# Kernel tuning notes

Hardware: AMD Instinct MI355X
Metric: run time of the kernel (lower is better)

Reference implementation:

```python
import jax, jax.numpy as jnp
import numpy as np

WINDOW_SIZE = 11
SIGMA = 1.5
C_IN = 3

def _gaussian_window():
    coords = jnp.arange(WINDOW_SIZE, dtype=jnp.float32) - WINDOW_SIZE // 2
    g = jnp.exp(-(coords ** 2) / (2.0 * SIGMA ** 2))
    g = g / g.sum()
    win = g[:, None] * g[None, :]                       # [11, 11]
    return jnp.broadcast_to(win[None, None], (C_IN, 1, WINDOW_SIZE, WINDOW_SIZE))

def _depthwise_conv(x, w):
    pad = WINDOW_SIZE // 2
    return jax.lax.conv_general_dilated(
        x, w,
        window_strides=(1, 1),
        padding=[(pad, pad), (pad, pad)],
        dimension_numbers=('NCHW', 'OIHW', 'NCHW'),
        feature_group_count=C_IN)

def setup_inputs() -> dict:
    key = jax.random.key(0)
    k1, k2 = jax.random.split(key)
    clean = jax.random.uniform(k1, (32, 3, 512, 512), dtype=jnp.float32)
    adversarial = jax.random.uniform(k2, (32, 3, 512, 512), dtype=jnp.float32)
    return {"clean": clean, "adversarial": adversarial}

def reference(clean, adversarial):
    C1 = 0.01 ** 2
    C2 = 0.03 ** 2
    w = _gaussian_window()
    mu1 = _depthwise_conv(clean, w)
    mu2 = _depthwise_conv(adversarial, w)
    mu1_sq = mu1 ** 2
    mu2_sq = mu2 ** 2
    mu12 = mu1 * mu2
    sigma1_sq = _depthwise_conv(clean ** 2, w) - mu1_sq
    sigma2_sq = _depthwise_conv(adversarial ** 2, w) - mu2_sq
    sigma12 = _depthwise_conv(clean * adversarial, w) - mu12
    ssim_map = ((2.0 * mu12 + C1) * (2.0 * sigma12 + C2)) / (
        (mu1_sq + mu2_sq + C1) * (sigma1_sq + sigma2_sq + C2))
    return 1.0 - ssim_map.mean()
```

## Files before the change

### kernel.cpp

```cpp
#include <hip/hip_runtime.h>


typedef float v2f __attribute__((ext_vector_type(2)));

#define IMG 512
#define TILE 64
#define HALO 5
#define LROWS 74
#define LCOLS 74
#define LSTRIDE 76
#define RPT 8
#define NPIX 25165824.0

__device__ __constant__ const float WT_[1] = {0.f};
#define W0 0.00102838f
#define W1 0.00759876f
#define W2 0.03600077f
#define W3 0.10936068f
#define W4 0.21300552f
#define W5 0.26601173f
__device__ constexpr float WT[11] = {W0, W1, W2, W3, W4, W5, W4, W3, W2, W1, W0};

__global__ __launch_bounds__(256, 3) void ssim_main(
    const float* __restrict__ clean,
    const float* __restrict__ adv,
    double* __restrict__ accum)
{
    __shared__ __align__(16) v2f tile[LROWS * LSTRIDE];
    __shared__ float wpart[4];

    const int tid = threadIdx.x;
    const int b = blockIdx.x;
    const int plane = b >> 6;
    const int t6 = b & 63;
    const int tile_x = (t6 & 7) * TILE;
    const int tile_y = (t6 >> 3) * TILE;

    const float* __restrict__ cp = clean + (size_t)plane * (IMG * IMG);
    const float* __restrict__ ap = adv   + (size_t)plane * (IMG * IMG);

    for (int idx = tid; idx < LROWS * LCOLS; idx += 256) {
        int r = idx / LCOLS;
        int c = idx - r * LCOLS;
        int gr = tile_y + r - HALO;
        int gc = tile_x + c - HALO;
        v2f v = {0.f, 0.f};
        if (gr >= 0 && gr < IMG && gc >= 0 && gc < IMG) {
            int gi = gr * IMG + gc;
            v.x = cp[gi];
            v.y = ap[gi];
        }
        tile[r * LSTRIDE + c] = v;
    }
    __syncthreads();

    const int cpair = tid & 31;
    const int trow = tid >> 5;
    const int r0 = trow * RPT;

    v2f amu0[RPT], amu1[RPT], app0[RPT], app1[RPT];
    float axy0[RPT], axy1[RPT];
    #pragma unroll
    for (int o = 0; o < RPT; ++o) {
        amu0[o] = (v2f){0.f, 0.f}; amu1[o] = (v2f){0.f, 0.f};
        app0[o] = (v2f){0.f, 0.f}; app1[o] = (v2f){0.f, 0.f};
        axy0[o] = 0.f; axy1[o] = 0.f;
    }

    #pragma unroll
    for (int j = 0; j < RPT + 10; ++j) {
        const v2f* __restrict__ rp = &tile[(r0 + j) * LSTRIDE + 2 * cpair];

        v2f tp[12];
        #pragma unroll
        for (int k = 0; k < 12; ++k) tp[k] = rp[k];

        v2f hmu0 = {0.f, 0.f}, hmu1 = {0.f, 0.f};
        v2f hpp0 = {0.f, 0.f}, hpp1 = {0.f, 0.f};
        float hxy0 = 0.f, hxy1 = 0.f;
        #pragma unroll
        for (int k = 0; k < 12; ++k) {
            v2f t = tp[k];
            v2f pp = t * t;
            float xy = t.x * t.y;
            if (k < 11) {
                const float w = WT[k];
                hmu0 += w * t; hpp0 += w * pp; hxy0 += w * xy;
            }
            if (k > 0) {
                const float w = WT[k - 1];
                hmu1 += w * t; hpp1 += w * pp; hxy1 += w * xy;
            }
        }

        #pragma unroll
        for (int o = 0; o < RPT; ++o) {
            const int kv = j - o;
            if (kv >= 0 && kv < 11) {
                const float w = WT[kv];
                amu0[o] += w * hmu0; amu1[o] += w * hmu1;
                app0[o] += w * hpp0; app1[o] += w * hpp1;
                axy0[o] += w * hxy0; axy1[o] += w * hxy1;
            }
        }
    }

    const float C1 = 1e-4f;
    const float C2 = 9e-4f;
    float lsum = 0.f;
    #pragma unroll
    for (int o = 0; o < RPT; ++o) {
        #pragma unroll
        for (int s = 0; s < 2; ++s) {
            v2f amu = s ? amu1[o] : amu0[o];
            v2f app = s ? app1[o] : app0[o];
            float exy = s ? axy1[o] : axy0[o];
            float mu1 = amu.x, mu2 = amu.y;
            float mu1s = mu1 * mu1;
            float mu2s = mu2 * mu2;
            float mu12 = mu1 * mu2;
            float s1 = app.x - mu1s;
            float s2 = app.y - mu2s;
            float s12 = exy - mu12;
            float num = (2.f * mu12 + C1) * (2.f * s12 + C2);
            float den = (mu1s + mu2s + C1) * (s1 + s2 + C2);
            lsum += num * __builtin_amdgcn_rcpf(den);
        }
    }

    #pragma unroll
    for (int off = 32; off > 0; off >>= 1)
        lsum += __shfl_down(lsum, off);
    const int lane = tid & 63;
    const int wave = tid >> 6;
    if (lane == 0) wpart[wave] = lsum;
    __syncthreads();
    if (tid == 0) {
        float bs = wpart[0] + wpart[1] + wpart[2] + wpart[3];
        atomicAdd(accum, (double)bs);
    }
}

__global__ void ssim_finalize(const double* __restrict__ accum,
                              float* __restrict__ out)
{
    if (threadIdx.x == 0) {
        out[0] = 1.f - (float)(accum[0] / NPIX);
    }
}

extern "C" void kernel_launch(void* const* d_in, const int* in_sizes, int n_in,
                              void* d_out, int out_size, void* d_ws, size_t ws_size,
                              hipStream_t stream)
{
    const float* clean = (const float*)d_in[0];
    const float* adv   = (const float*)d_in[1];
    float* out = (float*)d_out;
    double* accum = (double*)d_ws;

    hipMemsetAsync(accum, 0, sizeof(double), stream);

    const int nblocks = 96 * 64;
    ssim_main<<<nblocks, 256, 0, stream>>>(clean, adv, accum);
    ssim_finalize<<<1, 64, 0, stream>>>(accum, out);
}
```

Baseline: 330.1 us.

## Use sum/difference transform to cut SSIM conv channels and widen blocks

Stores x+y and x-y in the shared tile, so the five blurred statistics reduce to four (two means and two squared terms). The SSIM terms are then rebuilt algebraically from these. Blocks grow to 512 threads with 4 output rows per thread instead of 8, and tile rows are read as 128-bit vector loads. The aims are less FMA work per pixel, more waves per CU and wider LDS reads. In exchange, each block now computes the vertical halo for more strips, and the cancellation in the rebuilt terms may cost some precision.

```diff
diff --git a/kernel.cpp b/kernel.cpp
--- a/kernel.cpp
+++ b/kernel.cpp
@@ -2,6 +2,7 @@
 
 
 typedef float v2f __attribute__((ext_vector_type(2)));
+typedef float v4f __attribute__((ext_vector_type(4)));
 
 #define IMG 512
 #define TILE 64
@@ -9,25 +10,23 @@
 #define LROWS 74
 #define LCOLS 74
 #define LSTRIDE 76
-#define RPT 8
+#define LSTRIDE4 38
+#define RPT 4
 #define NPIX 25165824.0
 
-__device__ __constant__ const float WT_[1] = {0.f};
-#define W0 0.00102838f
-#define W1 0.00759876f
-#define W2 0.03600077f
-#define W3 0.10936068f
-#define W4 0.21300552f
-#define W5 0.26601173f
-__device__ constexpr float WT[11] = {W0, W1, W2, W3, W4, W5, W4, W3, W2, W1, W0};
+__device__ constexpr float WT[11] = {
+    0.00102838f, 0.00759876f, 0.03600077f, 0.10936068f, 0.21300552f,
+    0.26601173f,
+    0.21300552f, 0.10936068f, 0.03600077f, 0.00759876f, 0.00102838f};
 
-__global__ __launch_bounds__(256, 3) void ssim_main(
-    const float* __restrict__ clean,
-    const float* __restrict__ adv,
-    double* __restrict__ accum)
+__global__ __launch_bounds__(512)
+__attribute__((amdgpu_waves_per_eu(6, 6)))
+void ssim_main(const float* __restrict__ clean,
+               const float* __restrict__ adv,
+               double* __restrict__ accum)
 {
     __shared__ __align__(16) v2f tile[LROWS * LSTRIDE];
-    __shared__ float wpart[4];
+    __shared__ float wpart[8];
 
     const int tid = threadIdx.x;
     const int b = blockIdx.x;
@@ -39,7 +38,7 @@
     const float* __restrict__ cp = clean + (size_t)plane * (IMG * IMG);
     const float* __restrict__ ap = adv   + (size_t)plane * (IMG * IMG);
 
-    for (int idx = tid; idx < LROWS * LCOLS; idx += 256) {
+    for (int idx = tid; idx < LROWS * LCOLS; idx += 512) {
         int r = idx / LCOLS;
         int c = idx - r * LCOLS;
         int gr = tile_y + r - HALO;
@@ -47,49 +46,52 @@
         v2f v = {0.f, 0.f};
         if (gr >= 0 && gr < IMG && gc >= 0 && gc < IMG) {
             int gi = gr * IMG + gc;
-            v.x = cp[gi];
-            v.y = ap[gi];
+            float x = cp[gi];
+            float y = ap[gi];
+            v.x = x + y;
+            v.y = x - y;
         }
         tile[r * LSTRIDE + c] = v;
     }
     __syncthreads();
 
     const int cpair = tid & 31;
-    const int trow = tid >> 5;
-    const int r0 = trow * RPT;
+    const int strip = tid >> 5;
+    const int r0 = strip * RPT;
+    const v4f* __restrict__ tile4 = (const v4f*)tile;
 
-    v2f amu0[RPT], amu1[RPT], app0[RPT], app1[RPT];
-    float axy0[RPT], axy1[RPT];
+    v2f aA0[RPT], aA1[RPT], aB0[RPT], aB1[RPT];
     #pragma unroll
     for (int o = 0; o < RPT; ++o) {
-        amu0[o] = (v2f){0.f, 0.f}; amu1[o] = (v2f){0.f, 0.f};
-        app0[o] = (v2f){0.f, 0.f}; app1[o] = (v2f){0.f, 0.f};
-        axy0[o] = 0.f; axy1[o] = 0.f;
+        aA0[o] = (v2f){0.f, 0.f}; aA1[o] = (v2f){0.f, 0.f};
+        aB0[o] = (v2f){0.f, 0.f}; aB1[o] = (v2f){0.f, 0.f};
     }
 
     #pragma unroll
     for (int j = 0; j < RPT + 10; ++j) {
-        const v2f* __restrict__ rp = &tile[(r0 + j) * LSTRIDE + 2 * cpair];
+        const v4f* bp = tile4 + (r0 + j) * LSTRIDE4 + cpair;
+        v4f q0 = bp[0], q1 = bp[1], q2 = bp[2], q3 = bp[3], q4 = bp[4], q5 = bp[5];
+        v2f t[12];
+        t[0]  = (v2f){q0.x, q0.y}; t[1]  = (v2f){q0.z, q0.w};
+        t[2]  = (v2f){q1.x, q1.y}; t[3]  = (v2f){q1.z, q1.w};
+        t[4]  = (v2f){q2.x, q2.y}; t[5]  = (v2f){q2.z, q2.w};
+        t[6]  = (v2f){q3.x, q3.y}; t[7]  = (v2f){q3.z, q3.w};
+        t[8]  = (v2f){q4.x, q4.y}; t[9]  = (v2f){q4.z, q4.w};
+        t[10] = (v2f){q5.x, q5.y}; t[11] = (v2f){q5.z, q5.w};
 
-        v2f tp[12];
-        #pragma unroll
-        for (int k = 0; k < 12; ++k) tp[k] = rp[k];
-
-        v2f hmu0 = {0.f, 0.f}, hmu1 = {0.f, 0.f};
-        v2f hpp0 = {0.f, 0.f}, hpp1 = {0.f, 0.f};
-        float hxy0 = 0.f, hxy1 = 0.f;
+        v2f hA0 = {0.f, 0.f}, hA1 = {0.f, 0.f};
+        v2f hB0 = {0.f, 0.f}, hB1 = {0.f, 0.f};
         #pragma unroll
         for (int k = 0; k < 12; ++k) {
-            v2f t = tp[k];
-            v2f pp = t * t;
-            float xy = t.x * t.y;
+            v2f tv = t[k];
+            v2f pp = tv * tv;
             if (k < 11) {
                 const float w = WT[k];
-                hmu0 += w * t; hpp0 += w * pp; hxy0 += w * xy;
+                hA0 += w * tv; hB0 += w * pp;
             }
             if (k > 0) {
                 const float w = WT[k - 1];
-                hmu1 += w * t; hpp1 += w * pp; hxy1 += w * xy;
+                hA1 += w * tv; hB1 += w * pp;
             }
         }
 
@@ -98,9 +100,8 @@
             const int kv = j - o;
             if (kv >= 0 && kv < 11) {
                 const float w = WT[kv];
-                amu0[o] += w * hmu0; amu1[o] += w * hmu1;
-                app0[o] += w * hpp0; app1[o] += w * hpp1;
-                axy0[o] += w * hxy0; axy1[o] += w * hxy1;
+                aA0[o] += w * hA0; aA1[o] += w * hA1;
+                aB0[o] += w * hB0; aB1[o] += w * hB1;
             }
         }
     }
@@ -112,19 +113,17 @@
     for (int o = 0; o < RPT; ++o) {
         #pragma unroll
         for (int s = 0; s < 2; ++s) {
-            v2f amu = s ? amu1[o] : amu0[o];
-            v2f app = s ? app1[o] : app0[o];
-            float exy = s ? axy1[o] : axy0[o];
-            float mu1 = amu.x, mu2 = amu.y;
-            float mu1s = mu1 * mu1;
-            float mu2s = mu2 * mu2;
-            float mu12 = mu1 * mu2;
-            float s1 = app.x - mu1s;
-            float s2 = app.y - mu2s;
-            float s12 = exy - mu12;
-            float num = (2.f * mu12 + C1) * (2.f * s12 + C2);
-            float den = (mu1s + mu2s + C1) * (s1 + s2 + C2);
-            lsum += num * __builtin_amdgcn_rcpf(den);
+            v2f a  = s ? aA1[o] : aA0[o];
+            v2f bb = s ? aB1[o] : aB0[o];
+            float U = a.x * a.x;
+            float V = a.y * a.y;
+            float halfUmV = 0.5f * (U - V);
+            float halfUpV = 0.5f * (U + V);
+            float num1 = halfUmV + C1;
+            float num2 = 0.5f * (bb.x - bb.y) - halfUmV + C2;
+            float den1 = halfUpV + C1;
+            float den2 = 0.5f * (bb.x + bb.y) - halfUpV + C2;
+            lsum += (num1 * num2) * __builtin_amdgcn_rcpf(den1 * den2);
         }
     }
 
@@ -136,7 +135,9 @@
     if (lane == 0) wpart[wave] = lsum;
     __syncthreads();
     if (tid == 0) {
-        float bs = wpart[0] + wpart[1] + wpart[2] + wpart[3];
+        float bs = 0.f;
+        #pragma unroll
+        for (int w = 0; w < 8; ++w) bs += wpart[w];
         atomicAdd(accum, (double)bs);
     }
 }
@@ -161,6 +162,6 @@
     hipMemsetAsync(accum, 0, sizeof(double), stream);
 
     const int nblocks = 96 * 64;
-    ssim_main<<<nblocks, 256, 0, stream>>>(clean, adv, accum);
+    ssim_main<<<nblocks, 512, 0, stream>>>(clean, adv, accum);
     ssim_finalize<<<1, 64, 0, stream>>>(accum, out);
 }
```

Result: faster. 311.6 us (-5.6%).
